# Kernel optimization log

Measured on AMD Instinct MI355X. Metric: run time of the kernel, lower is better.

The kernel has to match this reference:

```python
import jax, jax.numpy as jnp
import numpy as np

BN_EPS = 1e-5


def _gru(x, Wih, Whh, bih, bhh):
    # x: [B,S,D]; Wih: [3H,D]; Whh: [3H,H]; PyTorch gate order (r, z, n)
    B, S, D = x.shape
    H = Whh.shape[1]
    xg = jnp.einsum('bsd,gd->bsg', x, Wih) + bih  # [B,S,3H] precomputed input gates

    def step(h, xg_t):
        hg = h @ Whh.T + bhh
        xr, xz, xn = jnp.split(xg_t, 3, axis=-1)
        hr, hz, hn = jnp.split(hg, 3, axis=-1)
        r = jax.nn.sigmoid(xr + hr)
        z = jax.nn.sigmoid(xz + hz)
        n = jnp.tanh(xn + r * hn)
        h_new = (1.0 - z) * n + z * h
        return h_new, h_new

    h0 = jnp.zeros((B, H), x.dtype)
    _, hs = jax.lax.scan(step, h0, jnp.swapaxes(xg, 0, 1))  # [S,B,H]
    return jnp.swapaxes(hs, 0, 1)


def _lstm(x, Wih, Whh, bih, bhh):
    # x: [B,S,D]; PyTorch gate order (i, f, g, o)
    B, S, D = x.shape
    H = Whh.shape[1]
    xg = jnp.einsum('bsd,gd->bsg', x, Wih) + bih  # [B,S,4H]

    def step(carry, xg_t):
        h, c = carry
        g = xg_t + h @ Whh.T + bhh
        i, f, gg, o = jnp.split(g, 4, axis=-1)
        i = jax.nn.sigmoid(i)
        f = jax.nn.sigmoid(f)
        gg = jnp.tanh(gg)
        o = jax.nn.sigmoid(o)
        c_new = f * c + i * gg
        h_new = o * jnp.tanh(c_new)
        return (h_new, c_new), h_new

    h0 = jnp.zeros((B, H), x.dtype)
    c0 = jnp.zeros((B, H), x.dtype)
    _, hs = jax.lax.scan(step, (h0, c0), jnp.swapaxes(xg, 0, 1))
    return jnp.swapaxes(hs, 0, 1)


def setup_inputs() -> dict:
    key = jax.random.key(0)
    B, S, D, H = 64, 512, 40, 512
    ks = jax.random.split(key, 16)
    s_in = 1.0 / np.sqrt(H)

    def u(k, shape):
        return jax.random.uniform(k, shape, jnp.float32, -s_in, s_in)

    inp = {
        'x': jax.random.normal(ks[0], (B, S, D), jnp.float32),
        # rec1: GRU
        'gru_Wih': u(ks[1], (3 * H, D)),
        'gru_Whh': u(ks[2], (3 * H, H)),
        'gru_bih': u(ks[3], (3 * H,)),
        'gru_bhh': u(ks[4], (3 * H,)),
        # rec2: LSTM over [x, ssr] -> input D+1
        'lstm_Wih': u(ks[5], (4 * H, D + 1)),
        'lstm_Whh': u(ks[6], (4 * H, H)),
        'lstm_bih': u(ks[7], (4 * H,)),
        'lstm_bhh': u(ks[8], (4 * H,)),
        # fc1/fc2/fc3: hidden -> 1
        'fc1_w': u(ks[9], (1, H)), 'fc1_b': u(ks[10], (1,)),
        'fc2_w': u(ks[11], (1, H)), 'fc2_b': u(ks[12], (1,)),
        'fc3_w': u(ks[13], (1, H)), 'fc3_b': u(ks[14], (1,)),
        # BatchNorm1d affine params
        'bn_gamma': jnp.ones((H,), jnp.float32),
        'bn_beta': jnp.zeros((H,), jnp.float32),
    }
    return inp


def reference(x, gru_Wih, gru_Whh, gru_bih, gru_bhh,
              lstm_Wih, lstm_Whh, lstm_bih, lstm_bhh,
              fc1_w, fc1_b, fc2_w, fc2_b, fc3_w, fc3_b,
              bn_gamma, bn_beta):
    B, S, D = x.shape
    o1 = _gru(x, gru_Wih, gru_Whh, gru_bih, gru_bhh)  # [B,S,H]
    # BatchNorm1d (training mode): per-channel stats over (batch, time)
    mean = jnp.mean(o1, axis=(0, 1))
    var = jnp.mean((o1 - mean) ** 2, axis=(0, 1))
    o1 = (o1 - mean) * jax.lax.rsqrt(var + BN_EPS) * bn_gamma + bn_beta
    # gated scalar channel (dropout p=0 is identity)
    sr = jax.nn.relu(o1 @ fc1_w.T + fc1_b)            # [B,S,1]
    w = jnp.abs(jax.nn.sigmoid(o1 @ fc2_w.T + fc2_b))  # [B,S,1]
    ssr = sr * (w + 1.0)                              # [B,S,1]
    x2 = jnp.concatenate([x, ssr], axis=2)            # [B,S,D+1]
    o2 = _lstm(x2, lstm_Wih, lstm_Whh, lstm_bih, lstm_bhh)
    out = jax.nn.relu(o2 @ fc3_w.T + fc3_b)           # [B,S,1]
    return out, ssr
```

## Files before the change

### kernel.cpp

```cpp
#include <hip/hip_runtime.h>
#include <stdint.h>

#define MB 16
#define GW 16
#define NU 32
#define HD 512
#define SEQ 512
#define DX 40

using short8 = __attribute__((ext_vector_type(8))) short;
using f32x4  = __attribute__((ext_vector_type(4))) float;

__device__ __forceinline__ unsigned short f2bf(float f) {
  uint32_t u = __builtin_bit_cast(uint32_t, f);
  u += 0x7fffu + ((u >> 16) & 1u);
  return (unsigned short)(u >> 16);
}
__device__ __forceinline__ float sigm(float x) { return 1.0f / (1.0f + __expf(-x)); }


__global__ __launch_bounds__(512, 2) void gru_kernel(
    const float* __restrict__ x, const float* __restrict__ Wih,
    const float* __restrict__ Whh, const float* __restrict__ bih,
    const float* __restrict__ bhh, unsigned* __restrict__ flags,
    unsigned short* __restrict__ hbuf, float* __restrict__ o1,
    float* __restrict__ stats)
{
  const int wg = blockIdx.x & (GW - 1);
  const int g  = blockIdx.x >> 4;
  const int tid = threadIdx.x;
  const int wave = tid >> 6;
  const int lane = tid & 63;
  const int u0 = wg * NU;
  const int bg = g * MB;

  __shared__ unsigned short h_s[MB][520];
  __shared__ unsigned short x_s[MB][72];
  __shared__ float gate_s[3][MB][NU];
  __shared__ float xn_s[MB][NU];

  for (int i = tid; i < MB * 32; i += 512) x_s[i >> 5][40 + (i & 31)] = 0;

  short8 bfrag[18];
  const int myGate = wave >> 1;
  const int ut = wave & 1;
  const int kq = (lane >> 4) * 8;
  if (wave < 6) {
    const int row = myGate * HD + u0 + ut * 16 + (lane & 15);
    for (int kt = 0; kt < 16; ++kt) {
      const float* p = Whh + (size_t)row * HD + kt * 32 + kq;
      short8 f;
#pragma unroll
      for (int j = 0; j < 8; ++j) f[j] = (short)f2bf(p[j]);
      bfrag[kt] = f;
    }
    for (int kt = 16; kt < 18; ++kt) {
      short8 f;
#pragma unroll
      for (int j = 0; j < 8; ++j) {
        int c = kt * 32 + kq + j - HD;
        float v = (myGate < 2 && c < DX) ? Wih[(size_t)row * DX + c] : 0.0f;
        f[j] = (short)f2bf(v);
      }
      bfrag[kt] = f;
    }
  } else {
    const int row = 2 * HD + u0 + (wave - 6) * 16 + (lane & 15);
    for (int kt = 0; kt < 2; ++kt) {
      short8 f;
#pragma unroll
      for (int j = 0; j < 8; ++j) {
        int c = kt * 32 + kq + j;
        f[j] = (short)((c < DX) ? f2bf(Wih[(size_t)row * DX + c]) : 0);
      }
      bfrag[kt] = f;
    }
  }

  const int sb = tid >> 5;
  const int su = tid & 31;
  float hprev = 0.0f, ssum = 0.0f, ssq = 0.0f;
  const float b_r  = bih[u0 + su] + bhh[u0 + su];
  const float b_z  = bih[HD + u0 + su] + bhh[HD + u0 + su];
  const float b_in = bih[2 * HD + u0 + su];
  const float b_hn = bhh[2 * HD + u0 + su];

  unsigned* gf = flags + g * GW * 16;
  unsigned* myProdFlag = gf + ((tid & 127) >> 3) * 16;

  for (int t = 0; t < SEQ; ++t) {
    const unsigned long long* hin64 =
        (const unsigned long long*)(hbuf + ((size_t)g * 2 + (t & 1)) * MB * HD);
    uint32_t* hout32 =
        (uint32_t*)(hbuf + ((size_t)g * 2 + ((t + 1) & 1)) * MB * HD);

    {
      while (__hip_atomic_load(myProdFlag, __ATOMIC_RELAXED,
                               __HIP_MEMORY_SCOPE_AGENT) < (unsigned)t)
        __builtin_amdgcn_s_sleep(1);
#pragma unroll
      for (int it = 0; it < 4; ++it) {
        int q = it * 512 + tid;
        unsigned long long v = __hip_atomic_load(hin64 + q, __ATOMIC_RELAXED,
                                                 __HIP_MEMORY_SCOPE_AGENT);
        *(unsigned long long*)(&h_s[q >> 7][(q & 127) * 4]) = v;
      }
    }
    {
      int b = tid >> 5, c = tid & 31;
      const float* xr = x + ((size_t)(bg + b) * SEQ + t) * DX;
      x_s[b][c] = f2bf(xr[c]);
      if (c < 8) x_s[b][32 + c] = f2bf(xr[32 + c]);
    }
    __syncthreads();

    if (wave < 6) {
      const int m = lane & 15;
      f32x4 acc = {0.f, 0.f, 0.f, 0.f};
#pragma unroll
      for (int kt = 0; kt < 16; ++kt) {
        short8 a = *(const short8*)(&h_s[m][kt * 32 + kq]);
        acc = __builtin_amdgcn_mfma_f32_16x16x32_bf16(a, bfrag[kt], acc, 0, 0, 0);
      }
      short8 ax0 = *(const short8*)(&x_s[m][kq]);
      short8 ax1 = *(const short8*)(&x_s[m][32 + kq]);
      acc = __builtin_amdgcn_mfma_f32_16x16x32_bf16(ax0, bfrag[16], acc, 0, 0, 0);
      acc = __builtin_amdgcn_mfma_f32_16x16x32_bf16(ax1, bfrag[17], acc, 0, 0, 0);
#pragma unroll
      for (int r = 0; r < 4; ++r)
        gate_s[myGate][(lane >> 4) * 4 + r][ut * 16 + (lane & 15)] = acc[r];
    } else {
      const int m = lane & 15;
      f32x4 acc = {0.f, 0.f, 0.f, 0.f};
      short8 ax0 = *(const short8*)(&x_s[m][kq]);
      short8 ax1 = *(const short8*)(&x_s[m][32 + kq]);
      acc = __builtin_amdgcn_mfma_f32_16x16x32_bf16(ax0, bfrag[0], acc, 0, 0, 0);
      acc = __builtin_amdgcn_mfma_f32_16x16x32_bf16(ax1, bfrag[1], acc, 0, 0, 0);
#pragma unroll
      for (int r = 0; r < 4; ++r)
        xn_s[(lane >> 4) * 4 + r][(wave - 6) * 16 + (lane & 15)] = acc[r];
    }
    __syncthreads();

    float r_ = sigm(gate_s[0][sb][su] + b_r);
    float z_ = sigm(gate_s[1][sb][su] + b_z);
    float n_ = tanhf(xn_s[sb][su] + b_in + r_ * (gate_s[2][sb][su] + b_hn));
    float h = (1.0f - z_) * n_ + z_ * hprev;
    hprev = h;
    ssum += h; ssq += h * h;
    {
      float hp = __shfl_xor(h, 1);
      if ((tid & 1) == 0) {
        uint32_t packed = (uint32_t)f2bf(h) | ((uint32_t)f2bf(hp) << 16);
        __hip_atomic_store(hout32 + ((sb * HD + u0 + su) >> 1), packed,
                           __ATOMIC_RELAXED, __HIP_MEMORY_SCOPE_AGENT);
      }
    }
    __syncthreads();

    if (tid == 0)
      __hip_atomic_store(gf + wg * 16, (unsigned)(t + 1), __ATOMIC_RELAXED,
                         __HIP_MEMORY_SCOPE_AGENT);
    o1[((size_t)(bg + sb) * SEQ + t) * HD + u0 + su] = h;
  }

  atomicAdd(&stats[u0 + su], ssum);
  atomicAdd(&stats[HD + u0 + su], ssq);
}

__global__ __launch_bounds__(512, 2) void lstm_kernel(
    const float* __restrict__ x, const float* __restrict__ Wih,
    const float* __restrict__ Whh, const float* __restrict__ bih,
    const float* __restrict__ bhh, const float* __restrict__ ssr,
    unsigned* __restrict__ flags, unsigned short* __restrict__ hbuf,
    float* __restrict__ o2)
{
  const int wg = blockIdx.x & (GW - 1);
  const int g  = blockIdx.x >> 4;
  const int tid = threadIdx.x;
  const int wave = tid >> 6;
  const int lane = tid & 63;
  const int u0 = wg * NU;
  const int bg = g * MB;

  __shared__ unsigned short h_s[MB][520];
  __shared__ unsigned short x_s[MB][72];
  __shared__ float gate_s[4][MB][NU];

  for (int i = tid; i < MB * 32; i += 512) x_s[i >> 5][40 + (i & 31)] = 0;

  short8 bfrag[18];
  const int myGate = wave >> 1;
  const int ut = wave & 1;
  const int kq = (lane >> 4) * 8;
  {
    const int row = myGate * HD + u0 + ut * 16 + (lane & 15);
    for (int kt = 0; kt < 16; ++kt) {
      const float* p = Whh + (size_t)row * HD + kt * 32 + kq;
      short8 f;
#pragma unroll
      for (int j = 0; j < 8; ++j) f[j] = (short)f2bf(p[j]);
      bfrag[kt] = f;
    }
    for (int kt = 16; kt < 18; ++kt) {
      short8 f;
#pragma unroll
      for (int j = 0; j < 8; ++j) {
        int c = kt * 32 + kq + j - HD;
        float v = (c < 41) ? Wih[(size_t)row * 41 + c] : 0.0f;
        f[j] = (short)f2bf(v);
      }
      bfrag[kt] = f;
    }
  }

  const int sb = tid >> 5;
  const int su = tid & 31;
  float creg = 0.0f;
  const float b_i = bih[u0 + su] + bhh[u0 + su];
  const float b_f = bih[HD + u0 + su] + bhh[HD + u0 + su];
  const float b_g = bih[2 * HD + u0 + su] + bhh[2 * HD + u0 + su];
  const float b_o = bih[3 * HD + u0 + su] + bhh[3 * HD + u0 + su];

  unsigned* gf = flags + g * GW * 16;
  unsigned* myProdFlag = gf + ((tid & 127) >> 3) * 16;

  for (int t = 0; t < SEQ; ++t) {
    const unsigned long long* hin64 =
        (const unsigned long long*)(hbuf + ((size_t)g * 2 + (t & 1)) * MB * HD);
    uint32_t* hout32 =
        (uint32_t*)(hbuf + ((size_t)g * 2 + ((t + 1) & 1)) * MB * HD);

    {
      while (__hip_atomic_load(myProdFlag, __ATOMIC_RELAXED,
                               __HIP_MEMORY_SCOPE_AGENT) < (unsigned)t)
        __builtin_amdgcn_s_sleep(1);
#pragma unroll
      for (int it = 0; it < 4; ++it) {
        int q = it * 512 + tid;
        unsigned long long v = __hip_atomic_load(hin64 + q, __ATOMIC_RELAXED,
                                                 __HIP_MEMORY_SCOPE_AGENT);
        *(unsigned long long*)(&h_s[q >> 7][(q & 127) * 4]) = v;
      }
    }
    {
      int b = tid >> 5, c = tid & 31;
      const float* xr = x + ((size_t)(bg + b) * SEQ + t) * DX;
      x_s[b][c] = f2bf(xr[c]);
      if (c < 8) x_s[b][32 + c] = f2bf(xr[32 + c]);
      if (c == 8) x_s[b][40] = f2bf(ssr[(size_t)(bg + b) * SEQ + t]);
    }
    __syncthreads();

    {
      const int m = lane & 15;
      f32x4 acc = {0.f, 0.f, 0.f, 0.f};
#pragma unroll
      for (int kt = 0; kt < 16; ++kt) {
        short8 a = *(const short8*)(&h_s[m][kt * 32 + kq]);
        acc = __builtin_amdgcn_mfma_f32_16x16x32_bf16(a, bfrag[kt], acc, 0, 0, 0);
      }
      short8 ax0 = *(const short8*)(&x_s[m][kq]);
      short8 ax1 = *(const short8*)(&x_s[m][32 + kq]);
      acc = __builtin_amdgcn_mfma_f32_16x16x32_bf16(ax0, bfrag[16], acc, 0, 0, 0);
      acc = __builtin_amdgcn_mfma_f32_16x16x32_bf16(ax1, bfrag[17], acc, 0, 0, 0);
#pragma unroll
      for (int r = 0; r < 4; ++r)
        gate_s[myGate][(lane >> 4) * 4 + r][ut * 16 + (lane & 15)] = acc[r];
    }
    __syncthreads();

    float gi = sigm(gate_s[0][sb][su] + b_i);
    float gf_ = sigm(gate_s[1][sb][su] + b_f);
    float gg = tanhf(gate_s[2][sb][su] + b_g);
    float go = sigm(gate_s[3][sb][su] + b_o);
    creg = gf_ * creg + gi * gg;
    float h = go * tanhf(creg);
    {
      float hp = __shfl_xor(h, 1);
      if ((tid & 1) == 0) {
        uint32_t packed = (uint32_t)f2bf(h) | ((uint32_t)f2bf(hp) << 16);
        __hip_atomic_store(hout32 + ((sb * HD + u0 + su) >> 1), packed,
                           __ATOMIC_RELAXED, __HIP_MEMORY_SCOPE_AGENT);
      }
    }
    __syncthreads();

    if (tid == 0)
      __hip_atomic_store(gf + wg * 16, (unsigned)(t + 1), __ATOMIC_RELAXED,
                         __HIP_MEMORY_SCOPE_AGENT);
    o2[((size_t)(bg + sb) * SEQ + t) * HD + u0 + su] = h;
  }
}

__global__ __launch_bounds__(512) void coef_kernel(
    const float* __restrict__ stats, const float* __restrict__ fc1_w,
    const float* __restrict__ fc1_b, const float* __restrict__ fc2_w,
    const float* __restrict__ fc2_b, const float* __restrict__ gamma,
    const float* __restrict__ beta, float* __restrict__ coef)
{
  __shared__ float r1[512], r2[512];
  const int j = threadIdx.x;
  const float inv_n = 1.0f / 32768.0f;
  float mean = stats[j] * inv_n;
  float var = stats[HD + j] * inv_n - mean * mean;
  float scale = gamma[j] * rsqrtf(var + 1e-5f);
  float shift = beta[j] - mean * scale;
  coef[j] = fc1_w[j] * scale;
  coef[HD + j] = fc2_w[j] * scale;
  r1[j] = fc1_w[j] * shift;
  r2[j] = fc2_w[j] * shift;
  __syncthreads();
  for (int s = 256; s > 0; s >>= 1) {
    if (j < s) { r1[j] += r1[j + s]; r2[j] += r2[j + s]; }
    __syncthreads();
  }
  if (j == 0) {
    coef[2 * HD] = r1[0] + fc1_b[0];
    coef[2 * HD + 1] = r2[0] + fc2_b[0];
  }
}

__global__ __launch_bounds__(256) void ssr_kernel(
    const float* __restrict__ o1, const float* __restrict__ coef,
    float* __restrict__ ssr_ws, float* __restrict__ dssr)
{
  const int row = blockIdx.x * 4 + (threadIdx.x >> 6);
  const int lane = threadIdx.x & 63;
  const float* p = o1 + (size_t)row * HD + lane * 8;
  float s1 = 0.f, s2 = 0.f;
#pragma unroll
  for (int j = 0; j < 8; ++j) {
    float v = p[j];
    s1 += v * coef[lane * 8 + j];
    s2 += v * coef[HD + lane * 8 + j];
  }
#pragma unroll
  for (int off = 32; off > 0; off >>= 1) {
    s1 += __shfl_down(s1, off);
    s2 += __shfl_down(s2, off);
  }
  if (lane == 0) {
    float sr = fmaxf(s1 + coef[2 * HD], 0.0f);
    float w = fabsf(sigm(s2 + coef[2 * HD + 1]));
    float v = sr * (1.0f + w);
    ssr_ws[row] = v;
    dssr[row] = v;
  }
}

__global__ __launch_bounds__(256) void out_kernel(
    const float* __restrict__ o2, const float* __restrict__ fc3_w,
    const float* __restrict__ fc3_b, float* __restrict__ dout)
{
  const int row = blockIdx.x * 4 + (threadIdx.x >> 6);
  const int lane = threadIdx.x & 63;
  const float* p = o2 + (size_t)row * HD + lane * 8;
  float s = 0.f;
#pragma unroll
  for (int j = 0; j < 8; ++j) s += p[j] * fc3_w[lane * 8 + j];
#pragma unroll
  for (int off = 32; off > 0; off >>= 1) s += __shfl_down(s, off);
  if (lane == 0) dout[row] = fmaxf(s + fc3_b[0], 0.0f);
}

extern "C" void kernel_launch(void* const* d_in, const int* in_sizes, int n_in,
                              void* d_out, int out_size, void* d_ws, size_t ws_size,
                              hipStream_t stream) {
  (void)in_sizes; (void)n_in; (void)out_size; (void)ws_size;
  const float* x    = (const float*)d_in[0];
  const float* gWih = (const float*)d_in[1];
  const float* gWhh = (const float*)d_in[2];
  const float* gbih = (const float*)d_in[3];
  const float* gbhh = (const float*)d_in[4];
  const float* lWih = (const float*)d_in[5];
  const float* lWhh = (const float*)d_in[6];
  const float* lbih = (const float*)d_in[7];
  const float* lbhh = (const float*)d_in[8];
  const float* fc1w = (const float*)d_in[9];
  const float* fc1b = (const float*)d_in[10];
  const float* fc2w = (const float*)d_in[11];
  const float* fc2b = (const float*)d_in[12];
  const float* fc3w = (const float*)d_in[13];
  const float* fc3b = (const float*)d_in[14];
  const float* gam  = (const float*)d_in[15];
  const float* bet  = (const float*)d_in[16];
  float* out = (float*)d_out;

  char* ws = (char*)d_ws;
  unsigned* flags_g = (unsigned*)(ws + 0);
  unsigned* flags_l = (unsigned*)(ws + 4096);
  float* stats      = (float*)(ws + 8192);
  float* coef       = (float*)(ws + 16384);
  float* ssr_ws     = (float*)(ws + 32768);
  unsigned short* hbuf_g = (unsigned short*)(ws + 262144);
  unsigned short* hbuf_l = (unsigned short*)(ws + 393216);
  float* o1 = (float*)(ws + 1048576);
  float* o2 = o1 + (size_t)64 * SEQ * HD;

  hipMemsetAsync(ws, 0, 12288, stream);
  hipMemsetAsync(ws + 262144, 0, 262144, stream);

  gru_kernel<<<dim3(64), dim3(512), 0, stream>>>(x, gWih, gWhh, gbih, gbhh,
                                                 flags_g, hbuf_g, o1, stats);
  coef_kernel<<<dim3(1), dim3(512), 0, stream>>>(stats, fc1w, fc1b, fc2w, fc2b,
                                                 gam, bet, coef);
  ssr_kernel<<<dim3(8192), dim3(256), 0, stream>>>(o1, coef, ssr_ws, out + 32768);
  lstm_kernel<<<dim3(64), dim3(512), 0, stream>>>(x, lWih, lWhh, lbih, lbhh, ssr_ws,
                                                  flags_l, hbuf_l, o2);
  out_kernel<<<dim3(8192), dim3(256), 0, stream>>>(o2, fc3w, fc3b, out);
}
```

Before: 3.240 ms.

## Replace per-step flag handshake with step-tagged hidden-state words

The separate producer flag and its extra barrier are replaced by packing the step counter into the upper 32 bits of every 64-bit hidden-state word. Consumers spin directly on the data words, reloading only the stale ones, so there is no flag-then-data round trip and no trailing __syncthreads before the flag store. The MFMA reduction is split into two independent accumulators to shorten the dependency chain, and launch bounds drop to one block per CU. The cost is twice the exchange traffic per step, a larger hbuf, and a correctness dependence on 64-bit atomic stores being seen as single units.

```diff
diff --git a/kernel.cpp b/kernel.cpp
--- a/kernel.cpp
+++ b/kernel.cpp
@@ -19,12 +19,11 @@
 __device__ __forceinline__ float sigm(float x) { return 1.0f / (1.0f + __expf(-x)); }
 
 
-__global__ __launch_bounds__(512, 2) void gru_kernel(
+__global__ __launch_bounds__(512, 1) void gru_kernel(
     const float* __restrict__ x, const float* __restrict__ Wih,
     const float* __restrict__ Whh, const float* __restrict__ bih,
-    const float* __restrict__ bhh, unsigned* __restrict__ flags,
-    unsigned short* __restrict__ hbuf, float* __restrict__ o1,
-    float* __restrict__ stats)
+    const float* __restrict__ bhh, unsigned long long* __restrict__ hbuf,
+    float* __restrict__ o1, float* __restrict__ stats)
 {
   const int wg = blockIdx.x & (GW - 1);
   const int g  = blockIdx.x >> 4;
@@ -85,25 +84,35 @@
   const float b_in = bih[2 * HD + u0 + su];
   const float b_hn = bhh[2 * HD + u0 + su];
 
-  unsigned* gf = flags + g * GW * 16;
-  unsigned* myProdFlag = gf + ((tid & 127) >> 3) * 16;
-
   for (int t = 0; t < SEQ; ++t) {
-    const unsigned long long* hin64 =
-        (const unsigned long long*)(hbuf + ((size_t)g * 2 + (t & 1)) * MB * HD);
-    uint32_t* hout32 =
-        (uint32_t*)(hbuf + ((size_t)g * 2 + ((t + 1) & 1)) * MB * HD);
-
-    {
-      while (__hip_atomic_load(myProdFlag, __ATOMIC_RELAXED,
-                               __HIP_MEMORY_SCOPE_AGENT) < (unsigned)t)
-        __builtin_amdgcn_s_sleep(1);
-#pragma unroll
-      for (int it = 0; it < 4; ++it) {
+    const unsigned long long* hin =
+        hbuf + ((size_t)g * 2 + (t & 1)) * 4096;
+    unsigned long long* hout =
+        hbuf + ((size_t)g * 2 + ((t + 1) & 1)) * 4096;
+
+    {
+      unsigned long long v[8];
+#pragma unroll
+      for (int it = 0; it < 8; ++it)
+        v[it] = __hip_atomic_load(hin + it * 512 + tid, __ATOMIC_RELAXED,
+                                  __HIP_MEMORY_SCOPE_AGENT);
+      const unsigned tagw = (unsigned)t;
+      for (;;) {
+        unsigned stale = 0;
+#pragma unroll
+        for (int it = 0; it < 8; ++it)
+          stale |= ((unsigned)(v[it] >> 32) != tagw) ? (1u << it) : 0u;
+        if (!stale) break;
+#pragma unroll
+        for (int it = 0; it < 8; ++it)
+          if (stale & (1u << it))
+            v[it] = __hip_atomic_load(hin + it * 512 + tid, __ATOMIC_RELAXED,
+                                      __HIP_MEMORY_SCOPE_AGENT);
+      }
+#pragma unroll
+      for (int it = 0; it < 8; ++it) {
         int q = it * 512 + tid;
-        unsigned long long v = __hip_atomic_load(hin64 + q, __ATOMIC_RELAXED,
-                                                 __HIP_MEMORY_SCOPE_AGENT);
-        *(unsigned long long*)(&h_s[q >> 7][(q & 127) * 4]) = v;
+        *(uint32_t*)(&h_s[q >> 8][(q & 255) * 2]) = (uint32_t)v[it];
       }
     }
     {
@@ -116,16 +125,19 @@
 
     if (wave < 6) {
       const int m = lane & 15;
-      f32x4 acc = {0.f, 0.f, 0.f, 0.f};
-#pragma unroll
-      for (int kt = 0; kt < 16; ++kt) {
-        short8 a = *(const short8*)(&h_s[m][kt * 32 + kq]);
-        acc = __builtin_amdgcn_mfma_f32_16x16x32_bf16(a, bfrag[kt], acc, 0, 0, 0);
+      f32x4 a0 = {0.f, 0.f, 0.f, 0.f}, a1 = {0.f, 0.f, 0.f, 0.f};
+#pragma unroll
+      for (int kt = 0; kt < 16; kt += 2) {
+        short8 ha0 = *(const short8*)(&h_s[m][kt * 32 + kq]);
+        short8 ha1 = *(const short8*)(&h_s[m][(kt + 1) * 32 + kq]);
+        a0 = __builtin_amdgcn_mfma_f32_16x16x32_bf16(ha0, bfrag[kt], a0, 0, 0, 0);
+        a1 = __builtin_amdgcn_mfma_f32_16x16x32_bf16(ha1, bfrag[kt + 1], a1, 0, 0, 0);
       }
       short8 ax0 = *(const short8*)(&x_s[m][kq]);
       short8 ax1 = *(const short8*)(&x_s[m][32 + kq]);
-      acc = __builtin_amdgcn_mfma_f32_16x16x32_bf16(ax0, bfrag[16], acc, 0, 0, 0);
-      acc = __builtin_amdgcn_mfma_f32_16x16x32_bf16(ax1, bfrag[17], acc, 0, 0, 0);
+      a0 = __builtin_amdgcn_mfma_f32_16x16x32_bf16(ax0, bfrag[16], a0, 0, 0, 0);
+      a1 = __builtin_amdgcn_mfma_f32_16x16x32_bf16(ax1, bfrag[17], a1, 0, 0, 0);
+      f32x4 acc = a0 + a1;
 #pragma unroll
       for (int r = 0; r < 4; ++r)
         gate_s[myGate][(lane >> 4) * 4 + r][ut * 16 + (lane & 15)] = acc[r];
@@ -151,16 +163,13 @@
     {
       float hp = __shfl_xor(h, 1);
       if ((tid & 1) == 0) {
-        uint32_t packed = (uint32_t)f2bf(h) | ((uint32_t)f2bf(hp) << 16);
-        __hip_atomic_store(hout32 + ((sb * HD + u0 + su) >> 1), packed,
+        unsigned long long packed =
+            (unsigned long long)((uint32_t)f2bf(h) | ((uint32_t)f2bf(hp) << 16)) |
+            ((unsigned long long)(unsigned)(t + 1) << 32);
+        __hip_atomic_store(hout + ((sb * HD + u0 + su) >> 1), packed,
                            __ATOMIC_RELAXED, __HIP_MEMORY_SCOPE_AGENT);
       }
     }
-    __syncthreads();
-
-    if (tid == 0)
-      __hip_atomic_store(gf + wg * 16, (unsigned)(t + 1), __ATOMIC_RELAXED,
-                         __HIP_MEMORY_SCOPE_AGENT);
     o1[((size_t)(bg + sb) * SEQ + t) * HD + u0 + su] = h;
   }
 
@@ -168,12 +177,11 @@
   atomicAdd(&stats[HD + u0 + su], ssq);
 }
 
-__global__ __launch_bounds__(512, 2) void lstm_kernel(
+__global__ __launch_bounds__(512, 1) void lstm_kernel(
     const float* __restrict__ x, const float* __restrict__ Wih,
     const float* __restrict__ Whh, const float* __restrict__ bih,
     const float* __restrict__ bhh, const float* __restrict__ ssr,
-    unsigned* __restrict__ flags, unsigned short* __restrict__ hbuf,
-    float* __restrict__ o2)
+    unsigned long long* __restrict__ hbuf, float* __restrict__ o2)
 {
   const int wg = blockIdx.x & (GW - 1);
   const int g  = blockIdx.x >> 4;
@@ -222,25 +230,35 @@
   const float b_g = bih[2 * HD + u0 + su] + bhh[2 * HD + u0 + su];
   const float b_o = bih[3 * HD + u0 + su] + bhh[3 * HD + u0 + su];
 
-  unsigned* gf = flags + g * GW * 16;
-  unsigned* myProdFlag = gf + ((tid & 127) >> 3) * 16;
-
   for (int t = 0; t < SEQ; ++t) {
-    const unsigned long long* hin64 =
-        (const unsigned long long*)(hbuf + ((size_t)g * 2 + (t & 1)) * MB * HD);
-    uint32_t* hout32 =
-        (uint32_t*)(hbuf + ((size_t)g * 2 + ((t + 1) & 1)) * MB * HD);
-
-    {
-      while (__hip_atomic_load(myProdFlag, __ATOMIC_RELAXED,
-                               __HIP_MEMORY_SCOPE_AGENT) < (unsigned)t)
-        __builtin_amdgcn_s_sleep(1);
-#pragma unroll
-      for (int it = 0; it < 4; ++it) {
+    const unsigned long long* hin =
+        hbuf + ((size_t)g * 2 + (t & 1)) * 4096;
+    unsigned long long* hout =
+        hbuf + ((size_t)g * 2 + ((t + 1) & 1)) * 4096;
+
+    {
+      unsigned long long v[8];
+#pragma unroll
+      for (int it = 0; it < 8; ++it)
+        v[it] = __hip_atomic_load(hin + it * 512 + tid, __ATOMIC_RELAXED,
+                                  __HIP_MEMORY_SCOPE_AGENT);
+      const unsigned tagw = (unsigned)t;
+      for (;;) {
+        unsigned stale = 0;
+#pragma unroll
+        for (int it = 0; it < 8; ++it)
+          stale |= ((unsigned)(v[it] >> 32) != tagw) ? (1u << it) : 0u;
+        if (!stale) break;
+#pragma unroll
+        for (int it = 0; it < 8; ++it)
+          if (stale & (1u << it))
+            v[it] = __hip_atomic_load(hin + it * 512 + tid, __ATOMIC_RELAXED,
+                                      __HIP_MEMORY_SCOPE_AGENT);
+      }
+#pragma unroll
+      for (int it = 0; it < 8; ++it) {
         int q = it * 512 + tid;
-        unsigned long long v = __hip_atomic_load(hin64 + q, __ATOMIC_RELAXED,
-                                                 __HIP_MEMORY_SCOPE_AGENT);
-        *(unsigned long long*)(&h_s[q >> 7][(q & 127) * 4]) = v;
+        *(uint32_t*)(&h_s[q >> 8][(q & 255) * 2]) = (uint32_t)v[it];
       }
     }
     {
@@ -254,16 +272,19 @@
 
     {
       const int m = lane & 15;
-      f32x4 acc = {0.f, 0.f, 0.f, 0.f};
-#pragma unroll
-      for (int kt = 0; kt < 16; ++kt) {
-        short8 a = *(const short8*)(&h_s[m][kt * 32 + kq]);
-        acc = __builtin_amdgcn_mfma_f32_16x16x32_bf16(a, bfrag[kt], acc, 0, 0, 0);
+      f32x4 a0 = {0.f, 0.f, 0.f, 0.f}, a1 = {0.f, 0.f, 0.f, 0.f};
+#pragma unroll
+      for (int kt = 0; kt < 16; kt += 2) {
+        short8 ha0 = *(const short8*)(&h_s[m][kt * 32 + kq]);
+        short8 ha1 = *(const short8*)(&h_s[m][(kt + 1) * 32 + kq]);
+        a0 = __builtin_amdgcn_mfma_f32_16x16x32_bf16(ha0, bfrag[kt], a0, 0, 0, 0);
+        a1 = __builtin_amdgcn_mfma_f32_16x16x32_bf16(ha1, bfrag[kt + 1], a1, 0, 0, 0);
       }
       short8 ax0 = *(const short8*)(&x_s[m][kq]);
       short8 ax1 = *(const short8*)(&x_s[m][32 + kq]);
-      acc = __builtin_amdgcn_mfma_f32_16x16x32_bf16(ax0, bfrag[16], acc, 0, 0, 0);
-      acc = __builtin_amdgcn_mfma_f32_16x16x32_bf16(ax1, bfrag[17], acc, 0, 0, 0);
+      a0 = __builtin_amdgcn_mfma_f32_16x16x32_bf16(ax0, bfrag[16], a0, 0, 0, 0);
+      a1 = __builtin_amdgcn_mfma_f32_16x16x32_bf16(ax1, bfrag[17], a1, 0, 0, 0);
+      f32x4 acc = a0 + a1;
 #pragma unroll
       for (int r = 0; r < 4; ++r)
         gate_s[myGate][(lane >> 4) * 4 + r][ut * 16 + (lane & 15)] = acc[r];
@@ -279,16 +300,13 @@
     {
       float hp = __shfl_xor(h, 1);
       if ((tid & 1) == 0) {
-        uint32_t packed = (uint32_t)f2bf(h) | ((uint32_t)f2bf(hp) << 16);
-        __hip_atomic_store(hout32 + ((sb * HD + u0 + su) >> 1), packed,
+        unsigned long long packed =
+            (unsigned long long)((uint32_t)f2bf(h) | ((uint32_t)f2bf(hp) << 16)) |
+            ((unsigned long long)(unsigned)(t + 1) << 32);
+        __hip_atomic_store(hout + ((sb * HD + u0 + su) >> 1), packed,
                            __ATOMIC_RELAXED, __HIP_MEMORY_SCOPE_AGENT);
       }
     }
-    __syncthreads();
-
-    if (tid == 0)
-      __hip_atomic_store(gf + wg * 16, (unsigned)(t + 1), __ATOMIC_RELAXED,
-                         __HIP_MEMORY_SCOPE_AGENT);
     o2[((size_t)(bg + sb) * SEQ + t) * HD + u0 + su] = h;
   }
 }
@@ -388,25 +406,23 @@
   float* out = (float*)d_out;
 
   char* ws = (char*)d_ws;
-  unsigned* flags_g = (unsigned*)(ws + 0);
-  unsigned* flags_l = (unsigned*)(ws + 4096);
   float* stats      = (float*)(ws + 8192);
   float* coef       = (float*)(ws + 16384);
   float* ssr_ws     = (float*)(ws + 32768);
-  unsigned short* hbuf_g = (unsigned short*)(ws + 262144);
-  unsigned short* hbuf_l = (unsigned short*)(ws + 393216);
+  unsigned long long* hbuf_g = (unsigned long long*)(ws + 262144);
+  unsigned long long* hbuf_l = (unsigned long long*)(ws + 524288);
   float* o1 = (float*)(ws + 1048576);
   float* o2 = o1 + (size_t)64 * SEQ * HD;
 
-  hipMemsetAsync(ws, 0, 12288, stream);
-  hipMemsetAsync(ws + 262144, 0, 262144, stream);
+  hipMemsetAsync(ws + 8192, 0, 4096, stream);
+  hipMemsetAsync(ws + 262144, 0, 524288, stream);
 
   gru_kernel<<<dim3(64), dim3(512), 0, stream>>>(x, gWih, gWhh, gbih, gbhh,
-                                                 flags_g, hbuf_g, o1, stats);
+                                                 hbuf_g, o1, stats);
   coef_kernel<<<dim3(1), dim3(512), 0, stream>>>(stats, fc1w, fc1b, fc2w, fc2b,
                                                  gam, bet, coef);
   ssr_kernel<<<dim3(8192), dim3(256), 0, stream>>>(o1, coef, ssr_ws, out + 32768);
   lstm_kernel<<<dim3(64), dim3(512), 0, stream>>>(x, lWih, lWhh, lbih, lbhh, ssr_ws,
-                                                  flags_l, hbuf_l, o2);
+                                                  hbuf_l, o2);
   out_kernel<<<dim3(8192), dim3(256), 0, stream>>>(o2, fc3w, fc3b, out);
 }
```

Result: slower. 3.559 ms (+9.8%).

## Split each batch group into two half-batches and ping-pong their recurrence steps

Applied to the files above, without the earlier changes.

Each workgroup's 16-row batch is split into two independent 8-row halves that alternate. While one half computes its gate MFMAs and activations, the other half's hidden-state exchange (flag wait and global load) is in flight, which hides the cross-workgroup sync latency. The MFMA k-loop also uses two accumulators to shorten the dependency chain. In exchange, half the MFMA rows are wasted because each 16-row tile now carries only 8 valid rows, there are more barriers per timestep, the flag and workspace layout changes, and the launch bounds drop to one block per SIMD.

```diff
diff --git a/kernel.cpp b/kernel.cpp
--- a/kernel.cpp
+++ b/kernel.cpp
@@ -7,6 +7,7 @@
 #define HD 512
 #define SEQ 512
 #define DX 40
+#define HB 8
 
 using short8 = __attribute__((ext_vector_type(8))) short;
 using f32x4  = __attribute__((ext_vector_type(4))) float;
@@ -18,12 +19,14 @@
 }
 __device__ __forceinline__ float sigm(float x) { return 1.0f / (1.0f + __expf(-x)); }
 
-
-__global__ __launch_bounds__(512, 2) void gru_kernel(
+#define MFMA_B16(a, b, c) __builtin_amdgcn_mfma_f32_16x16x32_bf16((a), (b), (c), 0, 0, 0)
+
+
+__global__ __launch_bounds__(512, 1) void gru_kernel(
     const float* __restrict__ x, const float* __restrict__ Wih,
     const float* __restrict__ Whh, const float* __restrict__ bih,
     const float* __restrict__ bhh, unsigned* __restrict__ flags,
-    unsigned short* __restrict__ hbuf, float* __restrict__ o1,
+    uint32_t* __restrict__ hbuf, float* __restrict__ o1,
     float* __restrict__ stats)
 {
   const int wg = blockIdx.x & (GW - 1);
@@ -34,12 +37,10 @@
   const int u0 = wg * NU;
   const int bg = g * MB;
 
-  __shared__ unsigned short h_s[MB][520];
-  __shared__ unsigned short x_s[MB][72];
-  __shared__ float gate_s[3][MB][NU];
-  __shared__ float xn_s[MB][NU];
-
-  for (int i = tid; i < MB * 32; i += 512) x_s[i >> 5][40 + (i & 31)] = 0;
+  __shared__ __align__(16) unsigned short h_s[2][HB][520];
+  __shared__ __align__(16) unsigned short x_s[2][HB][72];
+  __shared__ float gate_s[3][HB][NU];
+  __shared__ float xn_s[HB][NU];
 
   short8 bfrag[18];
   const int myGate = wave >> 1;
@@ -79,100 +80,129 @@
 
   const int sb = tid >> 5;
   const int su = tid & 31;
-  float hprev = 0.0f, ssum = 0.0f, ssq = 0.0f;
+  float hprevA = 0.f, hprevB = 0.f, ssum = 0.f, ssq = 0.f;
   const float b_r  = bih[u0 + su] + bhh[u0 + su];
   const float b_z  = bih[HD + u0 + su] + bhh[HD + u0 + su];
   const float b_in = bih[2 * HD + u0 + su];
   const float b_hn = bhh[2 * HD + u0 + su];
 
-  unsigned* gf = flags + g * GW * 16;
-  unsigned* myProdFlag = gf + ((tid & 127) >> 3) * 16;
+  unsigned* flagA = flags + (size_t)(g * 2 + 0) * GW * 16;
+  unsigned* flagB = flags + (size_t)(g * 2 + 1) * GW * 16;
+  const int prodIdx = (tid & 127) >> 3;
+
+  if (tid < 288) ((unsigned long long*)x_s)[tid] = 0ull;
+  __syncthreads();
+  {
+    *(unsigned long long*)(&h_s[0][tid >> 7][(tid & 127) * 4]) = 0ull;
+    int q = 512 + tid;
+    *(unsigned long long*)(&h_s[0][q >> 7][(q & 127) * 4]) = 0ull;
+    if (lane < 40)
+      x_s[0][wave][lane] = f2bf(x[((size_t)(bg + wave) * SEQ) * DX + lane]);
+  }
+  __syncthreads();
+
+#define GRU_SUB(H, O, T, TP, HPREV)                                           \
+  do {                                                                        \
+    if (wave < 6) {                                                           \
+      const int m = lane & 7;                                                 \
+      f32x4 a0 = {0.f, 0.f, 0.f, 0.f}, a1 = {0.f, 0.f, 0.f, 0.f};             \
+      _Pragma("unroll")                                                       \
+      for (int kt = 0; kt < 16; kt += 2) {                                    \
+        short8 ha0 = *(const short8*)(&h_s[H][m][kt * 32 + kq]);              \
+        short8 ha1 = *(const short8*)(&h_s[H][m][(kt + 1) * 32 + kq]);        \
+        a0 = MFMA_B16(ha0, bfrag[kt], a0);                                    \
+        a1 = MFMA_B16(ha1, bfrag[kt + 1], a1);                                \
+      }                                                                       \
+      short8 ax0 = *(const short8*)(&x_s[H][m][kq]);                          \
+      short8 ax1 = *(const short8*)(&x_s[H][m][32 + kq]);                     \
+      a0 = MFMA_B16(ax0, bfrag[16], a0);                                      \
+      a1 = MFMA_B16(ax1, bfrag[17], a1);                                      \
+      f32x4 acc = a0 + a1;                                                    \
+      if (lane < 32) {                                                        \
+        _Pragma("unroll")                                                     \
+        for (int r = 0; r < 4; ++r)                                           \
+          gate_s[myGate][(lane >> 4) * 4 + r][ut * 16 + (lane & 15)] = acc[r];\
+      }                                                                       \
+    } else {                                                                  \
+      const int m = lane & 7;                                                 \
+      f32x4 acc = {0.f, 0.f, 0.f, 0.f};                                       \
+      short8 ax0 = *(const short8*)(&x_s[H][m][kq]);                          \
+      short8 ax1 = *(const short8*)(&x_s[H][m][32 + kq]);                     \
+      acc = MFMA_B16(ax0, bfrag[0], acc);                                     \
+      acc = MFMA_B16(ax1, bfrag[1], acc);                                     \
+      if (lane < 32) {                                                        \
+        _Pragma("unroll")                                                     \
+        for (int r = 0; r < 4; ++r)                                           \
+          xn_s[(lane >> 4) * 4 + r][(wave - 6) * 16 + (lane & 15)] = acc[r];  \
+      }                                                                       \
+    }                                                                         \
+    __syncthreads();                                      \
+    unsigned long long pv0 = 0, pv1 = 0;                                      \
+    if ((TP) < SEQ) {                                                         \
+      unsigned* mf = ((O) ? flagB : flagA) + prodIdx * 16;                    \
+      while (__hip_atomic_load(mf, __ATOMIC_RELAXED,                          \
+                               __HIP_MEMORY_SCOPE_AGENT) < (unsigned)(TP))    \
+        __builtin_amdgcn_s_sleep(1);                                          \
+      const unsigned long long* hin = (const unsigned long long*)             \
+          (hbuf + ((size_t)g * 4 + (O) * 2 + ((TP) & 1)) * 2048);             \
+      pv0 = __hip_atomic_load(hin + tid, __ATOMIC_RELAXED,                    \
+                              __HIP_MEMORY_SCOPE_AGENT);                      \
+      pv1 = __hip_atomic_load(hin + 512 + tid, __ATOMIC_RELAXED,              \
+                              __HIP_MEMORY_SCOPE_AGENT);                      \
+    }                                                                         \
+    float hval = 0.f;                                                         \
+    if (tid < 256) {                                                          \
+      float r_ = sigm(gate_s[0][sb][su] + b_r);                               \
+      float z_ = sigm(gate_s[1][sb][su] + b_z);                               \
+      float n_ = tanhf(xn_s[sb][su] + b_in +                                  \
+                       r_ * (gate_s[2][sb][su] + b_hn));                      \
+      hval = (1.0f - z_) * n_ + z_ * (HPREV);                                 \
+      HPREV = hval;                                                           \
+      ssum += hval; ssq += hval * hval;                                       \
+      float hp = __shfl_xor(hval, 1);                                         \
+      if ((tid & 1) == 0) {                                                   \
+        uint32_t packed = (uint32_t)f2bf(hval) | ((uint32_t)f2bf(hp) << 16);  \
+        uint32_t* hout =                                                      \
+            hbuf + ((size_t)g * 4 + (H) * 2 + (((T) + 1) & 1)) * 2048;        \
+        __hip_atomic_store(hout + ((sb * HD + u0 + su) >> 1), packed,         \
+                           __ATOMIC_RELAXED, __HIP_MEMORY_SCOPE_AGENT);       \
+      }                                                                       \
+    }                                                                         \
+    __syncthreads();               \
+    if (tid == 0)                                                             \
+      __hip_atomic_store(((H) ? flagB : flagA) + wg * 16,                     \
+                         (unsigned)((T) + 1), __ATOMIC_RELAXED,               \
+                         __HIP_MEMORY_SCOPE_AGENT);                           \
+    if (tid < 256)                                                            \
+      o1[((size_t)(bg + (H) * HB + sb) * SEQ + (T)) * HD + u0 + su] = hval;   \
+    if ((TP) < SEQ) {                                                         \
+      *(unsigned long long*)(&h_s[O][tid >> 7][(tid & 127) * 4]) = pv0;       \
+      int q = 512 + tid;                                                      \
+      *(unsigned long long*)(&h_s[O][q >> 7][(q & 127) * 4]) = pv1;           \
+      if (lane < 40)                                                          \
+        x_s[O][wave][lane] = f2bf(                                            \
+            x[((size_t)(bg + (O) * HB + wave) * SEQ + (TP)) * DX + lane]);    \
+    }                                                                         \
+    __syncthreads();                             \
+  } while (0)
 
   for (int t = 0; t < SEQ; ++t) {
-    const unsigned long long* hin64 =
-        (const unsigned long long*)(hbuf + ((size_t)g * 2 + (t & 1)) * MB * HD);
-    uint32_t* hout32 =
-        (uint32_t*)(hbuf + ((size_t)g * 2 + ((t + 1) & 1)) * MB * HD);
-
-    {
-      while (__hip_atomic_load(myProdFlag, __ATOMIC_RELAXED,
-                               __HIP_MEMORY_SCOPE_AGENT) < (unsigned)t)
-        __builtin_amdgcn_s_sleep(1);
-#pragma unroll
-      for (int it = 0; it < 4; ++it) {
-        int q = it * 512 + tid;
-        unsigned long long v = __hip_atomic_load(hin64 + q, __ATOMIC_RELAXED,
-                                                 __HIP_MEMORY_SCOPE_AGENT);
-        *(unsigned long long*)(&h_s[q >> 7][(q & 127) * 4]) = v;
-      }
-    }
-    {
-      int b = tid >> 5, c = tid & 31;
-      const float* xr = x + ((size_t)(bg + b) * SEQ + t) * DX;
-      x_s[b][c] = f2bf(xr[c]);
-      if (c < 8) x_s[b][32 + c] = f2bf(xr[32 + c]);
-    }
-    __syncthreads();
-
-    if (wave < 6) {
-      const int m = lane & 15;
-      f32x4 acc = {0.f, 0.f, 0.f, 0.f};
-#pragma unroll
-      for (int kt = 0; kt < 16; ++kt) {
-        short8 a = *(const short8*)(&h_s[m][kt * 32 + kq]);
-        acc = __builtin_amdgcn_mfma_f32_16x16x32_bf16(a, bfrag[kt], acc, 0, 0, 0);
-      }
-      short8 ax0 = *(const short8*)(&x_s[m][kq]);
-      short8 ax1 = *(const short8*)(&x_s[m][32 + kq]);
-      acc = __builtin_amdgcn_mfma_f32_16x16x32_bf16(ax0, bfrag[16], acc, 0, 0, 0);
-      acc = __builtin_amdgcn_mfma_f32_16x16x32_bf16(ax1, bfrag[17], acc, 0, 0, 0);
-#pragma unroll
-      for (int r = 0; r < 4; ++r)
-        gate_s[myGate][(lane >> 4) * 4 + r][ut * 16 + (lane & 15)] = acc[r];
-    } else {
-      const int m = lane & 15;
-      f32x4 acc = {0.f, 0.f, 0.f, 0.f};
-      short8 ax0 = *(const short8*)(&x_s[m][kq]);
-      short8 ax1 = *(const short8*)(&x_s[m][32 + kq]);
-      acc = __builtin_amdgcn_mfma_f32_16x16x32_bf16(ax0, bfrag[0], acc, 0, 0, 0);
-      acc = __builtin_amdgcn_mfma_f32_16x16x32_bf16(ax1, bfrag[1], acc, 0, 0, 0);
-#pragma unroll
-      for (int r = 0; r < 4; ++r)
-        xn_s[(lane >> 4) * 4 + r][(wave - 6) * 16 + (lane & 15)] = acc[r];
-    }
-    __syncthreads();
-
-    float r_ = sigm(gate_s[0][sb][su] + b_r);
-    float z_ = sigm(gate_s[1][sb][su] + b_z);
-    float n_ = tanhf(xn_s[sb][su] + b_in + r_ * (gate_s[2][sb][su] + b_hn));
-    float h = (1.0f - z_) * n_ + z_ * hprev;
-    hprev = h;
-    ssum += h; ssq += h * h;
-    {
-      float hp = __shfl_xor(h, 1);
-      if ((tid & 1) == 0) {
-        uint32_t packed = (uint32_t)f2bf(h) | ((uint32_t)f2bf(hp) << 16);
-        __hip_atomic_store(hout32 + ((sb * HD + u0 + su) >> 1), packed,
-                           __ATOMIC_RELAXED, __HIP_MEMORY_SCOPE_AGENT);
-      }
-    }
-    __syncthreads();
-
-    if (tid == 0)
-      __hip_atomic_store(gf + wg * 16, (unsigned)(t + 1), __ATOMIC_RELAXED,
-                         __HIP_MEMORY_SCOPE_AGENT);
-    o1[((size_t)(bg + sb) * SEQ + t) * HD + u0 + su] = h;
-  }
-
-  atomicAdd(&stats[u0 + su], ssum);
-  atomicAdd(&stats[HD + u0 + su], ssq);
-}
-
-__global__ __launch_bounds__(512, 2) void lstm_kernel(
+    GRU_SUB(0, 1, t, t, hprevA);
+    GRU_SUB(1, 0, t, t + 1, hprevB);
+  }
+#undef GRU_SUB
+
+  if (tid < 256) {
+    atomicAdd(&stats[u0 + su], ssum);
+    atomicAdd(&stats[HD + u0 + su], ssq);
+  }
+}
+
+__global__ __launch_bounds__(512, 1) void lstm_kernel(
     const float* __restrict__ x, const float* __restrict__ Wih,
     const float* __restrict__ Whh, const float* __restrict__ bih,
     const float* __restrict__ bhh, const float* __restrict__ ssr,
-    unsigned* __restrict__ flags, unsigned short* __restrict__ hbuf,
+    unsigned* __restrict__ flags, uint32_t* __restrict__ hbuf,
     float* __restrict__ o2)
 {
   const int wg = blockIdx.x & (GW - 1);
@@ -183,11 +213,9 @@
   const int u0 = wg * NU;
   const int bg = g * MB;
 
-  __shared__ unsigned short h_s[MB][520];
-  __shared__ unsigned short x_s[MB][72];
-  __shared__ float gate_s[4][MB][NU];
-
-  for (int i = tid; i < MB * 32; i += 512) x_s[i >> 5][40 + (i & 31)] = 0;
+  __shared__ __align__(16) unsigned short h_s[2][HB][520];
+  __shared__ __align__(16) unsigned short x_s[2][HB][72];
+  __shared__ float gate_s[4][HB][NU];
 
   short8 bfrag[18];
   const int myGate = wave >> 1;
@@ -216,81 +244,109 @@
 
   const int sb = tid >> 5;
   const int su = tid & 31;
-  float creg = 0.0f;
+  float cregA = 0.f, cregB = 0.f;
   const float b_i = bih[u0 + su] + bhh[u0 + su];
   const float b_f = bih[HD + u0 + su] + bhh[HD + u0 + su];
   const float b_g = bih[2 * HD + u0 + su] + bhh[2 * HD + u0 + su];
   const float b_o = bih[3 * HD + u0 + su] + bhh[3 * HD + u0 + su];
 
-  unsigned* gf = flags + g * GW * 16;
-  unsigned* myProdFlag = gf + ((tid & 127) >> 3) * 16;
+  unsigned* flagA = flags + (size_t)(g * 2 + 0) * GW * 16;
+  unsigned* flagB = flags + (size_t)(g * 2 + 1) * GW * 16;
+  const int prodIdx = (tid & 127) >> 3;
+
+  if (tid < 288) ((unsigned long long*)x_s)[tid] = 0ull;
+  __syncthreads();
+  {
+    *(unsigned long long*)(&h_s[0][tid >> 7][(tid & 127) * 4]) = 0ull;
+    int q = 512 + tid;
+    *(unsigned long long*)(&h_s[0][q >> 7][(q & 127) * 4]) = 0ull;
+    if (lane < 40)
+      x_s[0][wave][lane] = f2bf(x[((size_t)(bg + wave) * SEQ) * DX + lane]);
+    else if (lane == 40)
+      x_s[0][wave][40] = f2bf(ssr[(size_t)(bg + wave) * SEQ]);
+  }
+  __syncthreads();
+
+#define LSTM_SUB(H, O, T, TP, CREG)                                           \
+  do {                                                                        \
+    {                                                                         \
+      const int m = lane & 7;                                                 \
+      f32x4 a0 = {0.f, 0.f, 0.f, 0.f}, a1 = {0.f, 0.f, 0.f, 0.f};             \
+      _Pragma("unroll")                                                       \
+      for (int kt = 0; kt < 16; kt += 2) {                                    \
+        short8 ha0 = *(const short8*)(&h_s[H][m][kt * 32 + kq]);              \
+        short8 ha1 = *(const short8*)(&h_s[H][m][(kt + 1) * 32 + kq]);        \
+        a0 = MFMA_B16(ha0, bfrag[kt], a0);                                    \
+        a1 = MFMA_B16(ha1, bfrag[kt + 1], a1);                                \
+      }                                                                       \
+      short8 ax0 = *(const short8*)(&x_s[H][m][kq]);                          \
+      short8 ax1 = *(const short8*)(&x_s[H][m][32 + kq]);                     \
+      a0 = MFMA_B16(ax0, bfrag[16], a0);                                      \
+      a1 = MFMA_B16(ax1, bfrag[17], a1);                                      \
+      f32x4 acc = a0 + a1;                                                    \
+      if (lane < 32) {                                                        \
+        _Pragma("unroll")                                                     \
+        for (int r = 0; r < 4; ++r)                                           \
+          gate_s[myGate][(lane >> 4) * 4 + r][ut * 16 + (lane & 15)] = acc[r];\
+      }                                                                       \
+    }                                                                         \
+    __syncthreads();                                                   \
+    unsigned long long pv0 = 0, pv1 = 0;                                      \
+    if ((TP) < SEQ) {                                                         \
+      unsigned* mf = ((O) ? flagB : flagA) + prodIdx * 16;                    \
+      while (__hip_atomic_load(mf, __ATOMIC_RELAXED,                          \
+                               __HIP_MEMORY_SCOPE_AGENT) < (unsigned)(TP))    \
+        __builtin_amdgcn_s_sleep(1);                                          \
+      const unsigned long long* hin = (const unsigned long long*)             \
+          (hbuf + ((size_t)g * 4 + (O) * 2 + ((TP) & 1)) * 2048);             \
+      pv0 = __hip_atomic_load(hin + tid, __ATOMIC_RELAXED,                    \
+                              __HIP_MEMORY_SCOPE_AGENT);                      \
+      pv1 = __hip_atomic_load(hin + 512 + tid, __ATOMIC_RELAXED,              \
+                              __HIP_MEMORY_SCOPE_AGENT);                      \
+    }                                                                         \
+    float hval = 0.f;                                                         \
+    if (tid < 256) {                                                          \
+      float gi  = sigm(gate_s[0][sb][su] + b_i);                              \
+      float gf_ = sigm(gate_s[1][sb][su] + b_f);                              \
+      float gg  = tanhf(gate_s[2][sb][su] + b_g);                             \
+      float go  = sigm(gate_s[3][sb][su] + b_o);                              \
+      CREG = gf_ * (CREG) + gi * gg;                                          \
+      hval = go * tanhf(CREG);                                                \
+      float hp = __shfl_xor(hval, 1);                                         \
+      if ((tid & 1) == 0) {                                                   \
+        uint32_t packed = (uint32_t)f2bf(hval) | ((uint32_t)f2bf(hp) << 16);  \
+        uint32_t* hout =                                                      \
+            hbuf + ((size_t)g * 4 + (H) * 2 + (((T) + 1) & 1)) * 2048;        \
+        __hip_atomic_store(hout + ((sb * HD + u0 + su) >> 1), packed,         \
+                           __ATOMIC_RELAXED, __HIP_MEMORY_SCOPE_AGENT);       \
+      }                                                                       \
+    }                                                                         \
+    __syncthreads();                                                   \
+    if (tid == 0)                                                             \
+      __hip_atomic_store(((H) ? flagB : flagA) + wg * 16,                     \
+                         (unsigned)((T) + 1), __ATOMIC_RELAXED,               \
+                         __HIP_MEMORY_SCOPE_AGENT);                           \
+    if (tid < 256)                                                            \
+      o2[((size_t)(bg + (H) * HB + sb) * SEQ + (T)) * HD + u0 + su] = hval;   \
+    if ((TP) < SEQ) {                                                         \
+      *(unsigned long long*)(&h_s[O][tid >> 7][(tid & 127) * 4]) = pv0;       \
+      int q = 512 + tid;                                                      \
+      *(unsigned long long*)(&h_s[O][q >> 7][(q & 127) * 4]) = pv1;           \
+      if (lane < 40)                                                          \
+        x_s[O][wave][lane] = f2bf(                                            \
+            x[((size_t)(bg + (O) * HB + wave) * SEQ + (TP)) * DX + lane]);    \
+      else if (lane == 40)                                                    \
+        x_s[O][wave][40] =                                                    \
+            f2bf(ssr[(size_t)(bg + (O) * HB + wave) * SEQ + (TP)]);           \
+    }                                                                         \
+    __syncthreads();                                                   \
+  } while (0)
 
   for (int t = 0; t < SEQ; ++t) {
-    const unsigned long long* hin64 =
-        (const unsigned long long*)(hbuf + ((size_t)g * 2 + (t & 1)) * MB * HD);
-    uint32_t* hout32 =
-        (uint32_t*)(hbuf + ((size_t)g * 2 + ((t + 1) & 1)) * MB * HD);
-
-    {
-      while (__hip_atomic_load(myProdFlag, __ATOMIC_RELAXED,
-                               __HIP_MEMORY_SCOPE_AGENT) < (unsigned)t)
-        __builtin_amdgcn_s_sleep(1);
-#pragma unroll
-      for (int it = 0; it < 4; ++it) {
-        int q = it * 512 + tid;
-        unsigned long long v = __hip_atomic_load(hin64 + q, __ATOMIC_RELAXED,
-                                                 __HIP_MEMORY_SCOPE_AGENT);
-        *(unsigned long long*)(&h_s[q >> 7][(q & 127) * 4]) = v;
-      }
-    }
-    {
-      int b = tid >> 5, c = tid & 31;
-      const float* xr = x + ((size_t)(bg + b) * SEQ + t) * DX;
-      x_s[b][c] = f2bf(xr[c]);
-      if (c < 8) x_s[b][32 + c] = f2bf(xr[32 + c]);
-      if (c == 8) x_s[b][40] = f2bf(ssr[(size_t)(bg + b) * SEQ + t]);
-    }
-    __syncthreads();
-
-    {
-      const int m = lane & 15;
-      f32x4 acc = {0.f, 0.f, 0.f, 0.f};
-#pragma unroll
-      for (int kt = 0; kt < 16; ++kt) {
-        short8 a = *(const short8*)(&h_s[m][kt * 32 + kq]);
-        acc = __builtin_amdgcn_mfma_f32_16x16x32_bf16(a, bfrag[kt], acc, 0, 0, 0);
-      }
-      short8 ax0 = *(const short8*)(&x_s[m][kq]);
-      short8 ax1 = *(const short8*)(&x_s[m][32 + kq]);
-      acc = __builtin_amdgcn_mfma_f32_16x16x32_bf16(ax0, bfrag[16], acc, 0, 0, 0);
-      acc = __builtin_amdgcn_mfma_f32_16x16x32_bf16(ax1, bfrag[17], acc, 0, 0, 0);
-#pragma unroll
-      for (int r = 0; r < 4; ++r)
-        gate_s[myGate][(lane >> 4) * 4 + r][ut * 16 + (lane & 15)] = acc[r];
-    }
-    __syncthreads();
-
-    float gi = sigm(gate_s[0][sb][su] + b_i);
-    float gf_ = sigm(gate_s[1][sb][su] + b_f);
-    float gg = tanhf(gate_s[2][sb][su] + b_g);
-    float go = sigm(gate_s[3][sb][su] + b_o);
-    creg = gf_ * creg + gi * gg;
-    float h = go * tanhf(creg);
-    {
-      float hp = __shfl_xor(h, 1);
-      if ((tid & 1) == 0) {
-        uint32_t packed = (uint32_t)f2bf(h) | ((uint32_t)f2bf(hp) << 16);
-        __hip_atomic_store(hout32 + ((sb * HD + u0 + su) >> 1), packed,
-                           __ATOMIC_RELAXED, __HIP_MEMORY_SCOPE_AGENT);
-      }
-    }
-    __syncthreads();
-
-    if (tid == 0)
-      __hip_atomic_store(gf + wg * 16, (unsigned)(t + 1), __ATOMIC_RELAXED,
-                         __HIP_MEMORY_SCOPE_AGENT);
-    o2[((size_t)(bg + sb) * SEQ + t) * HD + u0 + su] = h;
-  }
+    LSTM_SUB(0, 1, t, t, cregA);
+    LSTM_SUB(1, 0, t, t + 1, cregB);
+  }
+#undef LSTM_SUB
 }
 
 __global__ __launch_bounds__(512) void coef_kernel(
@@ -389,16 +445,16 @@
 
   char* ws = (char*)d_ws;
   unsigned* flags_g = (unsigned*)(ws + 0);
-  unsigned* flags_l = (unsigned*)(ws + 4096);
-  float* stats      = (float*)(ws + 8192);
-  float* coef       = (float*)(ws + 16384);
+  unsigned* flags_l = (unsigned*)(ws + 8192);
+  float* stats      = (float*)(ws + 16384);
+  float* coef       = (float*)(ws + 24576);
   float* ssr_ws     = (float*)(ws + 32768);
-  unsigned short* hbuf_g = (unsigned short*)(ws + 262144);
-  unsigned short* hbuf_l = (unsigned short*)(ws + 393216);
+  uint32_t* hbuf_g  = (uint32_t*)(ws + 262144);
+  uint32_t* hbuf_l  = (uint32_t*)(ws + 393216);
   float* o1 = (float*)(ws + 1048576);
   float* o2 = o1 + (size_t)64 * SEQ * HD;
 
-  hipMemsetAsync(ws, 0, 12288, stream);
+  hipMemsetAsync(ws, 0, 20480, stream);
   hipMemsetAsync(ws + 262144, 0, 262144, stream);
 
   gru_kernel<<<dim3(64), dim3(512), 0, stream>>>(x, gWih, gWhh, gbih, gbhh,
```

Measured after the change: 4.195 ms. 29.5% more time.
